# Kernel tuning notes

Hardware: AMD Instinct MI355X
Metric: run time of the kernel (lower is better)

Reference implementation:

```python
import jax, jax.numpy as jnp
import numpy as np


def setup_inputs() -> dict:
    key = jax.random.key(0)
    ks = jax.random.split(key, 6)
    B, S, D, H = 8, 1024, 1024, 16
    dk = D // H
    inputs = jax.random.normal(ks[0], (B, S, D), dtype=jnp.float32)
    mask = jnp.ones((B, S), dtype=jnp.float32)
    scale = 0.02
    W_q = jax.random.normal(ks[1], (H, D, dk), dtype=jnp.float32) * scale
    W_k = jax.random.normal(ks[2], (H, D, dk), dtype=jnp.float32) * scale
    W_v = jax.random.normal(ks[3], (D, D), dtype=jnp.float32) * scale
    W_o = jax.random.normal(ks[4], (D, D), dtype=jnp.float32) * scale
    return {"inputs": inputs, "mask": mask, "W_q": W_q, "W_k": W_k,
            "W_v": W_v, "W_o": W_o}


def reference(inputs, mask, W_q, W_k, W_v, W_o):
    B, S, D = inputs.shape
    H, _, dk = W_q.shape
    # combined causal + padding mask: 1.0 where attention is disallowed
    causal = 1.0 - jnp.tril(jnp.ones((S, S), dtype=jnp.float32))  # [S,S]
    input_mask = mask[:, None, :] * mask[:, :, None]              # [B,S,S]
    bad = jnp.maximum(causal[None, :, :], 1.0 - input_mask)       # [B,S,S]

    V = jnp.einsum('bsd,de->bse', inputs, W_v)                    # shared values
    Q = jnp.einsum('bsd,hdk->bhsk', inputs, W_q)
    K = jnp.einsum('bsd,hdk->bhsk', inputs, W_k)
    scores = jnp.einsum('bhqk,bhsk->bhqs', Q, K) / jnp.sqrt(jnp.float32(dk))
    scores = scores - bad[:, None, :, :] * 1e9
    attn = jax.nn.softmax(scores, axis=-1)                        # [B,H,S,S]
    attn_avg = jnp.mean(attn, axis=1)                             # [B,S,S]
    Hout = jnp.einsum('bqs,bse->bqe', attn_avg, V)
    output = jnp.einsum('bqe,ed->bqd', Hout, W_o)
    return (output, attn_avg)
```

## Files before the change

kernel.cpp:

```cpp
#include <hip/hip_runtime.h>

typedef unsigned short ushort;
typedef __bf16 bf16x8 __attribute__((ext_vector_type(8)));
typedef float f32x4 __attribute__((ext_vector_type(4)));
typedef unsigned short us8v __attribute__((ext_vector_type(8)));

__device__ __forceinline__ ushort f2bf(float f) {
  unsigned u = __builtin_bit_cast(unsigned, f);
  u += 0x7FFFu + ((u >> 16) & 1u);
  return (ushort)(u >> 16);
}

__device__ __forceinline__ bf16x8 ld_bf16x8(const ushort* p) {
  uint4 v = *(const uint4*)p;
  return __builtin_bit_cast(bf16x8, v);
}

__device__ __forceinline__ void gl16(const ushort* g, ushort* l) {
  __builtin_amdgcn_global_load_lds(
      (const __attribute__((address_space(1))) void*)g,
      (__attribute__((address_space(3))) void*)l, 16, 0, 0);
}

__global__ __launch_bounds__(256) void pack_x(const float* __restrict__ in,
                                              ushort* __restrict__ out) {
  long i = (long)blockIdx.x * 256 + threadIdx.x;
  const float4* s = (const float4*)in;
  float4 a = s[i * 2], b = s[i * 2 + 1];
  us8v o;
  o[0] = f2bf(a.x); o[1] = f2bf(a.y); o[2] = f2bf(a.z); o[3] = f2bf(a.w);
  o[4] = f2bf(b.x); o[5] = f2bf(b.y); o[6] = f2bf(b.z); o[7] = f2bf(b.w);
  *(us8v*)&out[i * 8] = o;
}

__global__ __launch_bounds__(256) void transpose_pack(
    const float* __restrict__ src, ushort* __restrict__ dst,
    int sC, int dLd, long sBatch, long dBatch, float scale) {
  src += (long)blockIdx.z * sBatch;
  dst += (long)blockIdx.z * dBatch;
  const int r0 = blockIdx.y * 64, c0 = blockIdx.x * 64;
  __shared__ ushort T[64 * 68];
  const int t = threadIdx.x;
#pragma unroll
  for (int i = 0; i < 4; ++i) {
    int ch = t + 256 * i;
    int r = ch >> 4, c4 = ch & 15;
    float4 v = *(const float4*)&src[(long)(r0 + r) * sC + c0 + c4 * 4];
    T[(c4 * 4 + 0) * 68 + r] = f2bf(v.x * scale);
    T[(c4 * 4 + 1) * 68 + r] = f2bf(v.y * scale);
    T[(c4 * 4 + 2) * 68 + r] = f2bf(v.z * scale);
    T[(c4 * 4 + 3) * 68 + r] = f2bf(v.w * scale);
  }
  __syncthreads();
#pragma unroll
  for (int i = 0; i < 4; ++i) {
    int ch = t + 256 * i;
    int c = ch >> 4, r4 = ch & 15;
    ushort4 o;
    o.x = T[c * 68 + r4 * 4 + 0];
    o.y = T[c * 68 + r4 * 4 + 1];
    o.z = T[c * 68 + r4 * 4 + 2];
    o.w = T[c * 68 + r4 * 4 + 3];
    *(ushort4*)&dst[(long)(c0 + c) * dLd + r0 + r4 * 4] = o;
  }
}

template <int EPI, bool CAUSAL, int SWZ>
__global__ __launch_bounds__(512, 1) void gemm3b(
    const ushort* __restrict__ A, const ushort* __restrict__ Bt,
    int N, int K, long aB, long bB,
    ushort* __restrict__ O_q, ushort* __restrict__ O_k, ushort* __restrict__ O_v,
    ushort* __restrict__ O_b, long oB,
    float* __restrict__ O_f) {
  __shared__ __align__(16) ushort As[3][256 * 64];
  __shared__ __align__(16) ushort Bs[3][128 * 64];
  const int tid = threadIdx.x;
  const int lane = tid & 63, w = tid >> 6;
  const int lr = lane & 15, lg = lane >> 4;

  const int nx = gridDim.x, ny = gridDim.y;
  long hw = blockIdx.x + (long)nx * (blockIdx.y + (long)ny * blockIdx.z);
  int k8 = (int)(hw & 7);
  long l = hw >> 3;
  int bx, by, z;
  if (SWZ == 1) {
    const int BH = ny >> 3;
    by = k8 * BH + (int)(l % BH);
    bx = (int)(l / BH);
    z = 0;
  } else {
    z = k8;
    by = (int)(l % ny);
    bx = (int)(l / ny);
  }

  const int row0 = by * 256, col0 = bx * 128;
  A += (long)z * aB;
  Bt += (long)z * bB;
  const int wr = (w >> 1) * 64, wc = (w & 1) * 64;

  f32x4 acc[4][4] = {};
  const int kmax = CAUSAL ? (K < row0 + 256 ? K : row0 + 256) : K;
  const int nk = kmax >> 6;

  auto stage = [&](int buf, int kt) {
    const int k0 = kt << 6;
#pragma unroll
    for (int j = 0; j < 4; ++j) {
      int c = tid + 512 * j;
      int r = c >> 3, c8 = (c & 7) ^ (r & 7);
      gl16(&A[(long)(row0 + r) * K + k0 + c8 * 8], &As[buf][c * 8]);
    }
#pragma unroll
    for (int j = 0; j < 2; ++j) {
      int c = tid + 512 * j;
      int r = c >> 3, c8 = (c & 7) ^ (r & 7);
      gl16(&Bt[(long)(col0 + r) * K + k0 + c8 * 8], &Bs[buf][c * 8]);
    }
  };
  auto compute = [&](int buf) {
#pragma unroll
    for (int kk = 0; kk < 2; ++kk) {
      bf16x8 af[4], bfr[4];
#pragma unroll
      for (int m = 0; m < 4; ++m) {
        int row = wr + m * 16 + lr;
        int c8 = (kk * 4 + lg) ^ (row & 7);
        af[m] = ld_bf16x8(&As[buf][row * 64 + c8 * 8]);
      }
#pragma unroll
      for (int n = 0; n < 4; ++n) {
        int row = wc + n * 16 + lr;
        int c8 = (kk * 4 + lg) ^ (row & 7);
        bfr[n] = ld_bf16x8(&Bs[buf][row * 64 + c8 * 8]);
      }
      __builtin_amdgcn_s_setprio(1);
#pragma unroll
      for (int m = 0; m < 4; ++m)
#pragma unroll
        for (int n = 0; n < 4; ++n)
          acc[m][n] = __builtin_amdgcn_mfma_f32_16x16x32_bf16(af[m], bfr[n], acc[m][n], 0, 0, 0);
      __builtin_amdgcn_s_setprio(0);
    }
  };

  stage(0, 0);
  stage(1, 1);
  asm volatile("s_waitcnt vmcnt(6)" ::: "memory");
  __builtin_amdgcn_s_barrier();
  __builtin_amdgcn_sched_barrier(0);
  for (int kt = 0; kt < nk; ++kt) {
    if (kt + 2 < nk) stage((kt + 2) % 3, kt + 2);
    compute(kt % 3);
    if (kt < nk - 1) {
      if (kt + 2 < nk) {
        asm volatile("s_waitcnt vmcnt(6)" ::: "memory");
      } else {
        asm volatile("s_waitcnt vmcnt(0)" ::: "memory");
      }
      __builtin_amdgcn_s_barrier();
      __builtin_amdgcn_sched_barrier(0);
    }
  }

#pragma unroll
  for (int m = 0; m < 4; ++m)
#pragma unroll
    for (int n = 0; n < 4; ++n)
#pragma unroll
      for (int r = 0; r < 4; ++r) {
        int gr = row0 + wr + m * 16 + lg * 4 + r;
        int gc = col0 + wc + n * 16 + lr;
        float v = acc[m][n][r];
        if (EPI == 0) {
          int b = gr >> 10, s = gr & 1023;
          if (gc < 1024) {
            int h = gc >> 6, kq = gc & 63;
            O_q[(((long)(b * 16 + h) << 10) + s) * 64 + kq] = f2bf(v);
          } else if (gc < 2048) {
            int n2 = gc - 1024;
            int h = n2 >> 6, kq = n2 & 63;
            O_k[(((long)(b * 16 + h) << 10) + s) * 64 + kq] = f2bf(v);
          } else {
            int e = gc - 2048;
            O_v[((long)(b << 10) + e) * 1024 + s] = f2bf(v);
          }
        } else if (EPI == 1) {
          (O_b + (long)z * oB)[(long)gr * N + gc] = f2bf(v);
        } else {
          O_f[(long)gr * N + gc] = v;
        }
      }
}

__global__ __launch_bounds__(512, 2) void attn16(
    const ushort* __restrict__ Qb, const ushort* __restrict__ Kb,
    const float* __restrict__ mask, float* __restrict__ attn_out,
    ushort* __restrict__ attnb) {
  __shared__ __align__(16) ushort Ks[2][4 * 128 * 64];
  __shared__ float redS[2][8][16];
  const int tid = threadIdx.x;
  const int lane = tid & 63, w = tid >> 6;
  const int lr = lane & 15, lg = lane >> 4;
  const int hw = blockIdx.x + 32 * blockIdx.y;
  const int b = hw & 7;
  const int x2 = hw >> 3;
  const int q0a = x2 * 16;
  const int q0b = (63 - x2) * 16;
  const int NTb = ((63 - x2) >> 3) + 1;
  const int n1 = (NTb - 4) << 10;
  const int NTWa = (x2 >> 4) * 2 + 2;
  const int NTWb = ((63 - x2) >> 4) * 2 + 2;

  float mqa[4], mqb[4], ms[8];
#pragma unroll
  for (int r = 0; r < 4; ++r) {
    mqa[r] = mask[b * 1024 + q0a + lg * 4 + r];
    mqb[r] = mask[b * 1024 + q0b + lg * 4 + r];
  }
#pragma unroll
  for (int t = 0; t < 8; ++t) ms[t] = mask[b * 1024 + t * 128 + w * 16 + lr];

  auto stageG = [&](int buf, int t0, int nch, int h) {
    const long hb = ((long)(b * 16 + h)) << 10;
#pragma unroll 2
    for (int i = tid; i < nch; i += 512) {
      int j = i >> 10, r = (i >> 3) & 127, c8 = i & 7;
      gl16(&Kb[(hb + (t0 + j) * 128 + r) * 64 + ((c8 ^ (r & 7)) << 3)],
           &Ks[buf][i * 8]);
    }
  };

  const int row = w * 16 + lr;
  const int cs0 = ((0 + lg) ^ (row & 7)) * 8;
  const int cs1 = ((4 + lg) ^ (row & 7)) * 8;

  stageG(0, 0, 4096, 0);
  __syncthreads();

  f32x4 acca[4] = {};
  f32x4 accb[8] = {};
#pragma unroll 1
  for (int h = 0; h < 16; ++h) {
    const long hb = ((long)(b * 16 + h)) << 10;
    const bf16x8 qa0 = ld_bf16x8(&Qb[(hb + q0a + lr) * 64 + lg * 8]);
    const bf16x8 qa1 = ld_bf16x8(&Qb[(hb + q0a + lr) * 64 + 32 + lg * 8]);
    const bf16x8 qb0 = ld_bf16x8(&Qb[(hb + q0b + lr) * 64 + lg * 8]);
    const bf16x8 qb1 = ld_bf16x8(&Qb[(hb + q0b + lr) * 64 + 32 + lg * 8]);

    stageG(1, 4, n1, h);

    f32x4 sca[4], scb[8];
    float psa[4] = {0.f, 0.f, 0.f, 0.f}, psb[4] = {0.f, 0.f, 0.f, 0.f};
#pragma unroll
    for (int t = 0; t < 4; ++t) {
      const int sb = t * 128 + w * 16;
      const ushort* kr = &Ks[0][(t * 128 + row) * 64];
      bf16x8 k0 = ld_bf16x8(kr + cs0);
      bf16x8 k1 = ld_bf16x8(kr + cs1);
      {
        f32x4 d = {};
        d = __builtin_amdgcn_mfma_f32_16x16x32_bf16(qb0, k0, d, 0, 0, 0);
        d = __builtin_amdgcn_mfma_f32_16x16x32_bf16(qb1, k1, d, 0, 0, 0);
#pragma unroll
        for (int r = 0; r < 4; ++r) {
          float e = __expf(d[r]) * (mqb[r] * ms[t]);
          scb[t][r] = e;
          psb[r] += e;
        }
      }
      if (sb <= q0a) {
        f32x4 d = {};
        d = __builtin_amdgcn_mfma_f32_16x16x32_bf16(qa0, k0, d, 0, 0, 0);
        d = __builtin_amdgcn_mfma_f32_16x16x32_bf16(qa1, k1, d, 0, 0, 0);
#pragma unroll
        for (int r = 0; r < 4; ++r) {
          float e = __expf(d[r]) * (mqa[r] * ms[t]);
          if (sb == q0a) e = (lr <= lg * 4 + r) ? e : 0.f;
          sca[t][r] = e;
          psa[r] += e;
        }
      }
    }
    __syncthreads();

    if (h < 15) stageG(0, 0, 4096, h + 1);

#pragma unroll
    for (int t = 4; t < 8; ++t) {
      const int sb = t * 128 + w * 16;
      if (sb <= q0b) {
        const ushort* kr = &Ks[1][((t - 4) * 128 + row) * 64];
        bf16x8 k0 = ld_bf16x8(kr + cs0);
        bf16x8 k1 = ld_bf16x8(kr + cs1);
        f32x4 d = {};
        d = __builtin_amdgcn_mfma_f32_16x16x32_bf16(qb0, k0, d, 0, 0, 0);
        d = __builtin_amdgcn_mfma_f32_16x16x32_bf16(qb1, k1, d, 0, 0, 0);
#pragma unroll
        for (int r = 0; r < 4; ++r) {
          float e = __expf(d[r]) * (mqb[r] * ms[t]);
          if (sb == q0b) e = (lr <= lg * 4 + r) ? e : 0.f;
          scb[t][r] = e;
          psb[r] += e;
        }
      }
    }
#pragma unroll
    for (int r = 0; r < 4; ++r) {
      psa[r] += __shfl_xor(psa[r], 1);
      psa[r] += __shfl_xor(psa[r], 2);
      psa[r] += __shfl_xor(psa[r], 4);
      psa[r] += __shfl_xor(psa[r], 8);
      psb[r] += __shfl_xor(psb[r], 1);
      psb[r] += __shfl_xor(psb[r], 2);
      psb[r] += __shfl_xor(psb[r], 4);
      psb[r] += __shfl_xor(psb[r], 8);
    }
    if (lr == 0) {
#pragma unroll
      for (int r = 0; r < 4; ++r) {
        redS[0][w][lg * 4 + r] = psa[r];
        redS[1][w][lg * 4 + r] = psb[r];
      }
    }
    __syncthreads();

#pragma unroll
    for (int r = 0; r < 4; ++r) {
      float ta = 0.f, tb = 0.f;
#pragma unroll
      for (int ww = 0; ww < 8; ++ww) {
        ta += redS[0][ww][lg * 4 + r];
        tb += redS[1][ww][lg * 4 + r];
      }
      float ra = __builtin_amdgcn_rcpf(ta);
      float rb = __builtin_amdgcn_rcpf(tb);
#pragma unroll
      for (int t = 0; t < 4; ++t) {
        const int sb = t * 128 + w * 16;
        if (sb <= q0a) acca[t][r] += sca[t][r] * ra;
      }
#pragma unroll
      for (int t = 0; t < 8; ++t) {
        const int sb = t * 128 + w * 16;
        if (sb <= q0b) accb[t][r] += scb[t][r] * rb;
      }
    }
  }

#pragma unroll
  for (int t = 0; t < 8; ++t) {
    int s = t * 128 + w * 16 + lr;
#pragma unroll
    for (int r = 0; r < 4; ++r) {
      {
        int q = q0a + lg * 4 + r;
        float v = (t < 4 ? acca[t][r] : 0.f) * 0.0625f;
        long o = ((long)(b * 1024 + q) << 10) + s;
        attn_out[o] = v;
        if (t < NTWa) attnb[o] = f2bf(v);
      }
      {
        int q = q0b + lg * 4 + r;
        float v = accb[t][r] * 0.0625f;
        long o = ((long)(b * 1024 + q) << 10) + s;
        attn_out[o] = v;
        if (t < NTWb) attnb[o] = f2bf(v);
      }
    }
  }
}

extern "C" void kernel_launch(void* const* d_in, const int* in_sizes, int n_in,
                              void* d_out, int out_size, void* d_ws, size_t ws_size,
                              hipStream_t stream) {
  const float* inputs = (const float*)d_in[0];
  const float* mask   = (const float*)d_in[1];
  const float* W_q    = (const float*)d_in[2];
  const float* W_k    = (const float*)d_in[3];
  const float* W_v    = (const float*)d_in[4];
  const float* W_o    = (const float*)d_in[5];
  float* out = (float*)d_out;

  ushort* Xb    = (ushort*)d_ws;
  ushort* WqkvT = Xb + 8192L * 1024;
  ushort* WoT   = WqkvT + 3072L * 1024;
  ushort* Qb    = WoT + 1024L * 1024;
  ushort* Kb    = Qb + 8L * 16 * 1024 * 64;
  ushort* Vt    = Kb + 8L * 16 * 1024 * 64;
  ushort* attnb = Vt + 8L * 1024 * 1024;
  ushort* Houtb = attnb + 8L * 1024 * 1024;

  pack_x<<<4096, 256, 0, stream>>>(inputs, Xb);
  transpose_pack<<<dim3(1, 16, 16), 256, 0, stream>>>(W_q, WqkvT, 64, 1024,
                                                      65536L, 64L * 1024, 0.125f);
  transpose_pack<<<dim3(1, 16, 16), 256, 0, stream>>>(W_k, WqkvT + 1024L * 1024, 64, 1024,
                                                      65536L, 64L * 1024, 1.0f);
  transpose_pack<<<dim3(16, 16, 1), 256, 0, stream>>>(W_v, WqkvT + 2048L * 1024, 1024, 1024,
                                                      0L, 0L, 1.0f);
  transpose_pack<<<dim3(16, 16, 1), 256, 0, stream>>>(W_o, WoT, 1024, 1024,
                                                      0L, 0L, 1.0f);
  gemm3b<0, false, 1><<<dim3(24, 32, 1), 512, 0, stream>>>(
      Xb, WqkvT, 3072, 1024, 0L, 0L, Qb, Kb, Vt, nullptr, 0L, nullptr);
  attn16<<<dim3(32, 8), 512, 0, stream>>>(Qb, Kb, mask, out + 8388608L, attnb);
  gemm3b<1, true, 0><<<dim3(8, 4, 8), 512, 0, stream>>>(
      attnb, Vt, 1024, 1024, 1048576L, 1048576L,
      nullptr, nullptr, nullptr, Houtb, 1048576L, nullptr);
  gemm3b<2, false, 1><<<dim3(8, 32, 1), 512, 0, stream>>>(
      Houtb, WoT, 1024, 1024, 0L, 0L,
      nullptr, nullptr, nullptr, nullptr, 0L, out);
}
```

Measured before the change: 235.6 us.

## Reassociate value and output projections into a fused Wv·Wo weight

Uses the identity output = attn_avg·(X·Wv)·Wo = (attn_avg·X)·(Wv·Wo). The combined weight Wv·Wo is built each call with a split-K GEMM, summed and packed to bf16. This removes the V columns from the QKV projection GEMM, and the attention-times-values GEMM now reads a transposed bf16 copy of the inputs. In exchange it adds a full transpose of X, a small 1024³ GEMM and a reduction kernel. The product weight is also rounded to bf16, which changes numerics slightly.

```diff
diff --git a/kernel.cpp b/kernel.cpp
--- a/kernel.cpp
+++ b/kernel.cpp
@@ -33,6 +33,20 @@
   *(us8v*)&out[i * 8] = o;
 }
 
+__global__ __launch_bounds__(256) void sum8_pack(const float* __restrict__ p,
+                                                 ushort* __restrict__ out) {
+  int i = (blockIdx.x * 256 + threadIdx.x) * 4;
+  float4 s = *(const float4*)&p[i];
+#pragma unroll
+  for (int z = 1; z < 8; ++z) {
+    float4 v = *(const float4*)&p[(long)z * 1048576 + i];
+    s.x += v.x; s.y += v.y; s.z += v.z; s.w += v.w;
+  }
+  ushort4 o;
+  o.x = f2bf(s.x); o.y = f2bf(s.y); o.z = f2bf(s.z); o.w = f2bf(s.w);
+  *(ushort4*)&out[i] = o;
+}
+
 __global__ __launch_bounds__(256) void transpose_pack(
     const float* __restrict__ src, ushort* __restrict__ dst,
     int sC, int dLd, long sBatch, long dBatch, float scale) {
@@ -65,11 +79,11 @@
   }
 }
 
-template <int EPI, bool CAUSAL, int SWZ>
+template <int EPI, bool CAUSAL, int SWZ, int KSPLIT>
 __global__ __launch_bounds__(512, 1) void gemm3b(
     const ushort* __restrict__ A, const ushort* __restrict__ Bt,
     int N, int K, long aB, long bB,
-    ushort* __restrict__ O_q, ushort* __restrict__ O_k, ushort* __restrict__ O_v,
+    ushort* __restrict__ O_q, ushort* __restrict__ O_k,
     ushort* __restrict__ O_b, long oB,
     float* __restrict__ O_f) {
   __shared__ __align__(16) ushort As[3][256 * 64];
@@ -101,7 +115,7 @@
 
   f32x4 acc[4][4] = {};
   const int kmax = CAUSAL ? (K < row0 + 256 ? K : row0 + 256) : K;
-  const int nk = kmax >> 6;
+  const int nk = (kmax >> 6) / KSPLIT;
 
   auto stage = [&](int buf, int kt) {
     const int k0 = kt << 6;
@@ -177,18 +191,15 @@
           if (gc < 1024) {
             int h = gc >> 6, kq = gc & 63;
             O_q[(((long)(b * 16 + h) << 10) + s) * 64 + kq] = f2bf(v);
-          } else if (gc < 2048) {
+          } else {
             int n2 = gc - 1024;
             int h = n2 >> 6, kq = n2 & 63;
             O_k[(((long)(b * 16 + h) << 10) + s) * 64 + kq] = f2bf(v);
-          } else {
-            int e = gc - 2048;
-            O_v[((long)(b << 10) + e) * 1024 + s] = f2bf(v);
           }
         } else if (EPI == 1) {
           (O_b + (long)z * oB)[(long)gr * N + gc] = f2bf(v);
         } else {
-          O_f[(long)gr * N + gc] = v;
+          (O_f + (long)z * oB)[(long)gr * N + gc] = v;
         }
       }
 }
@@ -383,30 +394,36 @@
   float* out = (float*)d_out;
 
   ushort* Xb    = (ushort*)d_ws;
-  ushort* WqkvT = Xb + 8192L * 1024;
-  ushort* WoT   = WqkvT + 3072L * 1024;
-  ushort* Qb    = WoT + 1024L * 1024;
+  ushort* XbT   = Xb + 8192L * 1024;
+  ushort* WqkT  = XbT + 8192L * 1024;
+  ushort* WoT   = WqkT + 2048L * 1024;
+  ushort* WvoT  = WoT + 1024L * 1024;
+  ushort* Qb    = WvoT + 1024L * 1024;
   ushort* Kb    = Qb + 8L * 16 * 1024 * 64;
-  ushort* Vt    = Kb + 8L * 16 * 1024 * 64;
-  ushort* attnb = Vt + 8L * 1024 * 1024;
-  ushort* Houtb = attnb + 8L * 1024 * 1024;
+  ushort* attnb = Kb + 8L * 16 * 1024 * 64;
+  ushort* H2b   = attnb + 8L * 1024 * 1024;
+  ushort* Wvb = Qb;
+  float* WvoP = (float*)attnb;
 
   pack_x<<<4096, 256, 0, stream>>>(inputs, Xb);
-  transpose_pack<<<dim3(1, 16, 16), 256, 0, stream>>>(W_q, WqkvT, 64, 1024,
+  transpose_pack<<<dim3(16, 16, 8), 256, 0, stream>>>(inputs, XbT, 1024, 1024,
+                                                      1048576L, 1048576L, 1.0f);
+  transpose_pack<<<dim3(1, 16, 16), 256, 0, stream>>>(W_q, WqkT, 64, 1024,
                                                       65536L, 64L * 1024, 0.125f);
-  transpose_pack<<<dim3(1, 16, 16), 256, 0, stream>>>(W_k, WqkvT + 1024L * 1024, 64, 1024,
+  transpose_pack<<<dim3(1, 16, 16), 256, 0, stream>>>(W_k, WqkT + 1024L * 1024, 64, 1024,
                                                       65536L, 64L * 1024, 1.0f);
-  transpose_pack<<<dim3(16, 16, 1), 256, 0, stream>>>(W_v, WqkvT + 2048L * 1024, 1024, 1024,
-                                                      0L, 0L, 1.0f);
   transpose_pack<<<dim3(16, 16, 1), 256, 0, stream>>>(W_o, WoT, 1024, 1024,
                                                       0L, 0L, 1.0f);
-  gemm3b<0, false, 1><<<dim3(24, 32, 1), 512, 0, stream>>>(
-      Xb, WqkvT, 3072, 1024, 0L, 0L, Qb, Kb, Vt, nullptr, 0L, nullptr);
+  pack_x<<<512, 256, 0, stream>>>(W_v, Wvb);
+  gemm3b<2, false, 0, 8><<<dim3(8, 4, 8), 512, 0, stream>>>(
+      WoT, Wvb, 1024, 1024, 128L, 128L, nullptr, nullptr, nullptr, 1048576L, WvoP);
+  sum8_pack<<<1024, 256, 0, stream>>>(WvoP, WvoT);
+  gemm3b<0, false, 1, 1><<<dim3(16, 32, 1), 512, 0, stream>>>(
+      Xb, WqkT, 2048, 1024, 0L, 0L, Qb, Kb, nullptr, 0L, nullptr);
   attn16<<<dim3(32, 8), 512, 0, stream>>>(Qb, Kb, mask, out + 8388608L, attnb);
-  gemm3b<1, true, 0><<<dim3(8, 4, 8), 512, 0, stream>>>(
-      attnb, Vt, 1024, 1024, 1048576L, 1048576L,
-      nullptr, nullptr, nullptr, Houtb, 1048576L, nullptr);
-  gemm3b<2, false, 1><<<dim3(8, 32, 1), 512, 0, stream>>>(
-      Houtb, WoT, 1024, 1024, 0L, 0L,
-      nullptr, nullptr, nullptr, nullptr, 0L, out);
-}
+  gemm3b<1, true, 0, 1><<<dim3(8, 4, 8), 512, 0, stream>>>(
+      attnb, XbT, 1024, 1024, 1048576L, 1048576L,
+      nullptr, nullptr, H2b, 1048576L, nullptr);
+  gemm3b<2, false, 1, 1><<<dim3(8, 32, 1), 512, 0, stream>>>(
+      H2b, WvoT, 1024, 1024, 0L, 0L, nullptr, nullptr, nullptr, 0L, out);
+}
```

Result: faster. 225.2 us (-4.4%).
